# Optimization experiments

Measured on AMD Instinct MI355X. Metric: run time of the kernel, lower is better.

The kernel has to match this reference:

```python
import jax, jax.numpy as jnp
import numpy as np

NU, NM = 100000, 20000   # users, merchants
FU, FM = 64, 32          # input feature dims
H = 128                  # hidden_channels
E = 1000000              # edges per edge type
ET = 500000              # target edges


def setup_inputs() -> dict:
    key = jax.random.key(0)
    ks = jax.random.split(key, 24)
    f = lambda i, shape: jax.random.normal(ks[i], shape, jnp.float32) * 0.05
    ri = lambda i, n, hi: jax.random.randint(ks[i], (n,), 0, hi)
    return {
        'x_user': f(0, (NU, FU)),
        'x_merchant': f(1, (NM, FM)),
        'row_um': ri(2, E, NU), 'col_um': ri(3, E, NM),
        'row_mu': ri(4, E, NM), 'col_mu': ri(5, E, NU),
        'row_t': ri(6, ET, NU), 'col_t': ri(7, ET, NM),
        'W1l_um': f(8, (FU, H)), 'W1r_um': f(9, (FM, H)), 'b1_um': jnp.zeros((H,), jnp.float32),
        'W1l_mu': f(10, (FM, H)), 'W1r_mu': f(11, (FU, H)), 'b1_mu': jnp.zeros((H,), jnp.float32),
        'W2l_um': f(12, (H, H)), 'W2r_um': f(13, (H, H)), 'b2_um': jnp.zeros((H,), jnp.float32),
        'W2l_mu': f(14, (H, H)), 'W2r_mu': f(15, (H, H)), 'b2_mu': jnp.zeros((H,), jnp.float32),
        'Wc1': f(16, (2 * H, H)), 'bc1': jnp.zeros((H,), jnp.float32),
        'Wc2': f(17, (H, 1)), 'bc2': jnp.zeros((1,), jnp.float32),
    }


def _sage(x_src, x_dst, row, col, Wl, Wr, b, n_dst):
    # PyG SAGEConv (aggr='mean'): lin_l(mean of neighbor msgs) + lin_r(root) + bias
    deg = jax.ops.segment_sum(jnp.ones(row.shape[0], x_src.dtype), col, num_segments=n_dst)
    agg = jax.ops.segment_sum(x_src[row], col, num_segments=n_dst)
    agg = agg / jnp.maximum(deg, 1.0)[:, None]
    return agg @ Wl + x_dst @ Wr + b


def reference(x_user, x_merchant, row_um, col_um, row_mu, col_mu, row_t, col_t,
              W1l_um, W1r_um, b1_um, W1l_mu, W1r_mu, b1_mu,
              W2l_um, W2r_um, b2_um, W2l_mu, W2r_mu, b2_mu,
              Wc1, bc1, Wc2, bc2):
    # Layer 1 (each dest type receives exactly one edge type -> hetero-mean is identity)
    h_m = jax.nn.relu(_sage(x_user, x_merchant, row_um, col_um, W1l_um, W1r_um, b1_um, NM))
    h_u = jax.nn.relu(_sage(x_merchant, x_user, row_mu, col_mu, W1l_mu, W1r_mu, b1_mu, NU))
    # Layer 2 (no activation)
    z_m = _sage(h_u, h_m, row_um, col_um, W2l_um, W2r_um, b2_um, NM)
    z_u = _sage(h_m, h_u, row_mu, col_mu, W2l_mu, W2r_mu, b2_mu, NU)
    # Edge classifier: gather sender ('user') / receiver ('merchant'), concat, MLP
    z = jnp.concatenate([z_u[row_t], z_m[col_t]], axis=-1)  # [ET, 2H]
    h = jax.nn.relu(z @ Wc1 + bc1)
    return (h @ Wc2 + bc2).reshape(-1)
```

## Files before the change

### kernel.cpp

```cpp
#include <hip/hip_runtime.h>
#include <hip/hip_bf16.h>

#define NUV 100000
#define NMV 20000
#define NEV 1000000
#define ETV 500000

#define REP 8
#define SCH2 16384
#define NCA 10
#define NCB 49
#define HGRID 1954
#define MBLK 5000
#define G1MB 625
#define G2MB 313

typedef unsigned short u16;
typedef unsigned int u32;
typedef __attribute__((ext_vector_type(8))) short s16x8;
typedef __attribute__((ext_vector_type(4))) float f32x4;
typedef __attribute__((ext_vector_type(4))) unsigned short u16x4;
typedef __attribute__((ext_vector_type(4))) unsigned int u32x4;

__device__ inline u16 bf16r(float f) {
  u32 b = __builtin_bit_cast(u32, f);
  u32 r = b + 0x7fffu + ((b >> 16) & 1u);
  return (u16)(r >> 16);
}
__device__ inline float bflo(u32 v) { return __builtin_bit_cast(float, v << 16); }
__device__ inline float bfhi(u32 v) { return __builtin_bit_cast(float, v & 0xffff0000u); }

__device__ inline int xcc_id() {
  unsigned x;
  asm volatile("s_getreg_b32 %0, hwreg(HW_REG_XCC_ID, 0, 8)" : "=s"(x));
  return (int)(x & 7u);
}

#define GLOAD_LDS16(src, dst) \
  __builtin_amdgcn_global_load_lds((const __attribute__((address_space(1))) void*)(src), \
                                   (__attribute__((address_space(3))) void*)(dst), 16, 0, 0)

__global__ __launch_bounds__(256) void k_hist_rank_p(
    const int* __restrict__ col_um, int* __restrict__ cnt_um, int* __restrict__ rank_um,
    const int* __restrict__ col_mu, int* __restrict__ cnt_mu, int* __restrict__ rank_mu) {
  int i = (blockIdx.x * 256 + threadIdx.x) * 4;
  if (i >= 2 * NEV) return;
  int r = xcc_id();
  u32 rtag = (u32)r << 24;
  bool um = i < NEV;
  const int* col = um ? col_um : col_mu;
  int* cnt = um ? cnt_um : cnt_mu;
  int* rank = um ? rank_um : rank_mu;
  int lo = um ? i : i - NEV;
  int4 c = *(const int4*)(col + lo);
  u32 k0 = (u32)__hip_atomic_fetch_add(&cnt[c.x * REP + r], 1, __ATOMIC_RELAXED, __HIP_MEMORY_SCOPE_WORKGROUP);
  u32 k1 = (u32)__hip_atomic_fetch_add(&cnt[c.y * REP + r], 1, __ATOMIC_RELAXED, __HIP_MEMORY_SCOPE_WORKGROUP);
  u32 k2 = (u32)__hip_atomic_fetch_add(&cnt[c.z * REP + r], 1, __ATOMIC_RELAXED, __HIP_MEMORY_SCOPE_WORKGROUP);
  u32 k3 = (u32)__hip_atomic_fetch_add(&cnt[c.w * REP + r], 1, __ATOMIC_RELAXED, __HIP_MEMORY_SCOPE_WORKGROUP);
  int4 k;
  k.x = (int)(k0 | rtag); k.y = (int)(k1 | rtag);
  k.z = (int)(k2 | rtag); k.w = (int)(k3 | rtag);
  *(int4*)(rank + lo) = k;
}

__global__ __launch_bounds__(1024) void k_scan_p1(const int* __restrict__ cntA, int nA,
                                                  const int* __restrict__ cntB, int nB,
                                                  int* __restrict__ bsum) {
  int b = blockIdx.x;
  const int* arr; int n; int c;
  if (b < NCA) { arr = cntA; n = nA; c = b; }
  else         { arr = cntB; n = nB; c = b - NCA; }
  __shared__ int wsum[16];
  int tid = threadIdx.x, lane = tid & 63, w = tid >> 6;
  int base = c * SCH2 + tid * 16;
  int s = 0;
  #pragma unroll
  for (int q = 0; q < 16; q += 4) {
    if (base + q + 3 < n) {
      int4 v = *(const int4*)(arr + base + q);
      s += v.x + v.y + v.z + v.w;
    } else {
      #pragma unroll
      for (int j = 0; j < 4; ++j) s += (base + q + j < n) ? arr[base + q + j] : 0;
    }
  }
  #pragma unroll
  for (int d = 1; d < 64; d <<= 1) s += __shfl_xor(s, d);
  if (lane == 0) wsum[w] = s;
  __syncthreads();
  if (tid == 0) {
    int tot = 0;
    #pragma unroll
    for (int j = 0; j < 16; ++j) tot += wsum[j];
    bsum[b] = tot;
  }
}

__global__ __launch_bounds__(128) void k_scan_p2(int* __restrict__ bsum,
                                                 int* __restrict__ off_um, int* __restrict__ off_mu) {
  int tid = threadIdx.x;
  int wv = tid >> 6, lane = tid & 63;
  if (wv == 0) {
    int v = (lane < NCA) ? bsum[lane] : 0;
    int s = v;
    #pragma unroll
    for (int d = 1; d < 64; d <<= 1) { int t = __shfl_up(s, d); if (lane >= d) s += t; }
    if (lane < NCA) bsum[lane] = s - v;
  } else {
    int v = (lane < NCB) ? bsum[NCA + lane] : 0;
    int s = v;
    #pragma unroll
    for (int d = 1; d < 64; d <<= 1) { int t = __shfl_up(s, d); if (lane >= d) s += t; }
    if (lane < NCB) bsum[NCA + lane] = s - v;
  }
  if (tid == 0) { off_um[NMV] = NEV; off_mu[NUV] = NEV; }
}

__global__ __launch_bounds__(1024) void k_scan_p3(int* __restrict__ cntA, int nA, int* __restrict__ offA,
                                                  int* __restrict__ cntB, int nB, int* __restrict__ offB,
                                                  const int* __restrict__ bsum) {
  int b = blockIdx.x;
  int* arr; int n; int c; int* offo;
  if (b < NCA) { arr = cntA; n = nA; c = b; offo = offA; }
  else         { arr = cntB; n = nB; c = b - NCA; offo = offB; }
  int carry = bsum[b];
  __shared__ int wsum[16];
  int tid = threadIdx.x, lane = tid & 63, w = tid >> 6;
  int base = c * SCH2 + tid * 16;
  int v[16];
  #pragma unroll
  for (int q = 0; q < 16; q += 4) {
    if (base + q + 3 < n) {
      int4 t = *(const int4*)(arr + base + q);
      v[q] = t.x; v[q + 1] = t.y; v[q + 2] = t.z; v[q + 3] = t.w;
    } else {
      #pragma unroll
      for (int j = 0; j < 4; ++j) v[q + j] = (base + q + j < n) ? arr[base + q + j] : 0;
    }
  }
  int tsum = 0;
  #pragma unroll
  for (int q = 0; q < 16; ++q) tsum += v[q];
  int sc = tsum;
  #pragma unroll
  for (int d = 1; d < 64; d <<= 1) { int t = __shfl_up(sc, d); if (lane >= d) sc += t; }
  if (lane == 63) wsum[w] = sc;
  __syncthreads();
  if (w == 0 && lane < 16) {
    int ws_ = wsum[lane];
    #pragma unroll
    for (int d = 1; d < 16; d <<= 1) { int t = __shfl_up(ws_, d, 16); if (lane >= d) ws_ += t; }
    wsum[lane] = ws_;
  }
  __syncthreads();
  int run = sc - tsum + (w ? wsum[w - 1] : 0) + carry;
  #pragma unroll
  for (int q = 0; q < 16; ++q) {
    int idx = base + q;
    if (idx < n) {
      arr[idx] = run;
      if ((idx & (REP - 1)) == 0) offo[idx / REP] = run;
      run += v[q];
    }
  }
}

__global__ __launch_bounds__(256) void k_scatter2(
    const int* __restrict__ col_um, const int* __restrict__ row_um,
    const int* __restrict__ rank_um, const int* __restrict__ base_um, int* __restrict__ srow_um,
    const int* __restrict__ col_mu, const int* __restrict__ row_mu,
    const int* __restrict__ rank_mu, const int* __restrict__ base_mu, int* __restrict__ srow_mu) {
  int i = (blockIdx.x * 256 + threadIdx.x) * 4;
  if (i >= 2 * NEV) return;
  bool um = i < NEV;
  const int* col = um ? col_um : col_mu;
  const int* row = um ? row_um : row_mu;
  const int* rank = um ? rank_um : rank_mu;
  const int* basep = um ? base_um : base_mu;
  int* srow = um ? srow_um : srow_mu;
  int lo = um ? i : i - NEV;
  int4 c = *(const int4*)(col + lo);
  int4 rr = *(const int4*)(row + lo);
  int4 k = *(const int4*)(rank + lo);
  u32 kx = (u32)k.x, ky = (u32)k.y, kz = (u32)k.z, kw = (u32)k.w;
  srow[basep[c.x * REP + (kx >> 24)] + (int)(kx & 0xFFFFFF)] = rr.x;
  srow[basep[c.y * REP + (ky >> 24)] + (int)(ky & 0xFFFFFF)] = rr.y;
  srow[basep[c.z * REP + (kz >> 24)] + (int)(kz & 0xFFFFFF)] = rr.z;
  srow[basep[c.w * REP + (kw >> 24)] + (int)(kw & 0xFFFFFF)] = rr.w;
}

__global__ __launch_bounds__(256) void k_xub(const float* __restrict__ in, u32* __restrict__ o, int n8) {
  int stride = gridDim.x * 256;
  for (int i = blockIdx.x * 256 + threadIdx.x; i < n8; i += stride) {
    float4 a = *(const float4*)(in + (size_t)i * 8);
    float4 b = *(const float4*)(in + (size_t)i * 8 + 4);
    u32x4 r;
    r[0] = (u32)bf16r(a.x) | ((u32)bf16r(a.y) << 16);
    r[1] = (u32)bf16r(a.z) | ((u32)bf16r(a.w) << 16);
    r[2] = (u32)bf16r(b.x) | ((u32)bf16r(b.y) << 16);
    r[3] = (u32)bf16r(b.z) | ((u32)bf16r(b.w) << 16);
    *(u32x4*)(o + (size_t)i * 4) = r;
  }
}

__global__ __launch_bounds__(256) void k_agg_l1(
    const int* __restrict__ off_um, const int* __restrict__ srow_um,
    const u32* __restrict__ xub, float* __restrict__ agg_m,
    const int* __restrict__ off_mu, const int* __restrict__ srow_mu,
    const float* __restrict__ xm, float* __restrict__ agg_u) {
  int bid = blockIdx.x, tid = threadIdx.x;
  int l = tid & 63, g = l >> 3, lr = l & 7;
  if (bid < MBLK) {
    int wid = (bid * 256 + tid) >> 6;
    int s = off_um[wid], t = off_um[wid + 1];
    float a[8] = {};
    int j = s;
    for (; j + 16 <= t; j += 16) {
      int r0 = srow_um[j + g], r1 = srow_um[j + 8 + g];
      u32x4 v0 = *(const u32x4*)(xub + (size_t)r0 * 32 + lr * 4);
      u32x4 v1 = *(const u32x4*)(xub + (size_t)r1 * 32 + lr * 4);
      #pragma unroll
      for (int k = 0; k < 4; ++k) {
        a[2 * k] += bflo(v0[k]) + bflo(v1[k]);
        a[2 * k + 1] += bfhi(v0[k]) + bfhi(v1[k]);
      }
    }
    for (; j + 8 <= t; j += 8) {
      int r0 = srow_um[j + g];
      u32x4 v0 = *(const u32x4*)(xub + (size_t)r0 * 32 + lr * 4);
      #pragma unroll
      for (int k = 0; k < 4; ++k) { a[2 * k] += bflo(v0[k]); a[2 * k + 1] += bfhi(v0[k]); }
    }
    if (g < t - j) {
      int r0 = srow_um[j + g];
      u32x4 v0 = *(const u32x4*)(xub + (size_t)r0 * 32 + lr * 4);
      #pragma unroll
      for (int k = 0; k < 4; ++k) { a[2 * k] += bflo(v0[k]); a[2 * k + 1] += bfhi(v0[k]); }
    }
    #pragma unroll
    for (int k = 0; k < 8; ++k) {
      a[k] += __shfl_xor(a[k], 8);
      a[k] += __shfl_xor(a[k], 16);
      a[k] += __shfl_xor(a[k], 32);
    }
    if (g == 0) {
      float inv = 1.f / (float)max(t - s, 1);
      float4 o0 = make_float4(a[0] * inv, a[1] * inv, a[2] * inv, a[3] * inv);
      float4 o1 = make_float4(a[4] * inv, a[5] * inv, a[6] * inv, a[7] * inv);
      *(float4*)(agg_m + (size_t)wid * 64 + lr * 8) = o0;
      *(float4*)(agg_m + (size_t)wid * 64 + lr * 8 + 4) = o1;
    }
  } else {
    int wid = ((bid - MBLK) * 256 + tid) >> 6;
    int s = off_mu[wid], t = off_mu[wid + 1];
    float a[4] = {};
    int j = s;
    for (; j + 16 <= t; j += 16) {
      int r0 = srow_mu[j + g], r1 = srow_mu[j + 8 + g];
      float4 v0 = *(const float4*)(xm + (size_t)r0 * 32 + lr * 4);
      float4 v1 = *(const float4*)(xm + (size_t)r1 * 32 + lr * 4);
      a[0] += v0.x + v1.x; a[1] += v0.y + v1.y;
      a[2] += v0.z + v1.z; a[3] += v0.w + v1.w;
    }
    for (; j + 8 <= t; j += 8) {
      int r0 = srow_mu[j + g];
      float4 v0 = *(const float4*)(xm + (size_t)r0 * 32 + lr * 4);
      a[0] += v0.x; a[1] += v0.y; a[2] += v0.z; a[3] += v0.w;
    }
    if (g < t - j) {
      int r0 = srow_mu[j + g];
      float4 v0 = *(const float4*)(xm + (size_t)r0 * 32 + lr * 4);
      a[0] += v0.x; a[1] += v0.y; a[2] += v0.z; a[3] += v0.w;
    }
    #pragma unroll
    for (int k = 0; k < 4; ++k) {
      a[k] += __shfl_xor(a[k], 8);
      a[k] += __shfl_xor(a[k], 16);
      a[k] += __shfl_xor(a[k], 32);
    }
    if (g == 0) {
      float inv = 1.f / (float)max(t - s, 1);
      *(float4*)(agg_u + (size_t)wid * 32 + lr * 4) =
          make_float4(a[0] * inv, a[1] * inv, a[2] * inv, a[3] * inv);
    }
  }
}

__global__ __launch_bounds__(256) void k_agg_l2(
    const int* __restrict__ off_um, const int* __restrict__ srow_um,
    const u16* __restrict__ h_u, u16* __restrict__ aggb_m,
    const int* __restrict__ off_mu, const int* __restrict__ srow_mu,
    const u16* __restrict__ h_m, u16* __restrict__ aggb_u) {
  int bid = blockIdx.x, tid = threadIdx.x;
  const int* off; const int* srow; const u32* x; u32* ag; int wid;
  if (bid < MBLK) {
    off = off_um; srow = srow_um; x = (const u32*)h_u; ag = (u32*)aggb_m;
    wid = (bid * 256 + tid) >> 6;
  } else {
    off = off_mu; srow = srow_mu; x = (const u32*)h_m; ag = (u32*)aggb_u;
    wid = ((bid - MBLK) * 256 + tid) >> 6;
  }
  int l = tid & 63, g = l >> 4, lr = l & 15;
  int s = off[wid], t = off[wid + 1];
  float a[8] = {};
  int j = s;
  for (; j + 8 <= t; j += 8) {
    int r0 = srow[j + g], r1 = srow[j + 4 + g];
    u32x4 v0 = *(const u32x4*)(x + (size_t)r0 * 64 + lr * 4);
    u32x4 v1 = *(const u32x4*)(x + (size_t)r1 * 64 + lr * 4);
    #pragma unroll
    for (int k = 0; k < 4; ++k) {
      a[2 * k] += bflo(v0[k]) + bflo(v1[k]);
      a[2 * k + 1] += bfhi(v0[k]) + bfhi(v1[k]);
    }
  }
  for (; j + 4 <= t; j += 4) {
    int r0 = srow[j + g];
    u32x4 v0 = *(const u32x4*)(x + (size_t)r0 * 64 + lr * 4);
    #pragma unroll
    for (int k = 0; k < 4; ++k) { a[2 * k] += bflo(v0[k]); a[2 * k + 1] += bfhi(v0[k]); }
  }
  if (g < t - j) {
    int r0 = srow[j + g];
    u32x4 v0 = *(const u32x4*)(x + (size_t)r0 * 64 + lr * 4);
    #pragma unroll
    for (int k = 0; k < 4; ++k) { a[2 * k] += bflo(v0[k]); a[2 * k + 1] += bfhi(v0[k]); }
  }
  #pragma unroll
  for (int k = 0; k < 8; ++k) {
    a[k] += __shfl_xor(a[k], 16);
    a[k] += __shfl_xor(a[k], 32);
  }
  if (g == 0) {
    float inv = 1.f / (float)max(t - s, 1);
    u32x4 o;
    #pragma unroll
    for (int k = 0; k < 4; ++k)
      o[k] = (u32)bf16r(a[2 * k] * inv) | ((u32)bf16r(a[2 * k + 1] * inv) << 16);
    *(u32x4*)(ag + (size_t)wid * 64 + lr * 4) = o;
  }
}

template <int KA, int KB>
__device__ inline void gemm1_body(const float* __restrict__ A, const float* __restrict__ B,
                                  const float* __restrict__ Wa, const float* __restrict__ Wb,
                                  const float* __restrict__ bias, u16* __restrict__ outb,
                                  int m0, float* At, float* Bt) {
  int tid = threadIdx.x;
  {
    int m = tid & 31, kq = tid >> 5;
    const float* Ar = A + (size_t)(m0 + m) * KA;
    for (int k0 = kq * 4; k0 < KA; k0 += 32) {
      float4 v = *(const float4*)(Ar + k0);
      At[(k0 + 0) * 32 + m] = v.x; At[(k0 + 1) * 32 + m] = v.y;
      At[(k0 + 2) * 32 + m] = v.z; At[(k0 + 3) * 32 + m] = v.w;
    }
    const float* Br = B + (size_t)(m0 + m) * KB;
    for (int k0 = kq * 4; k0 < KB; k0 += 32) {
      float4 v = *(const float4*)(Br + k0);
      Bt[(k0 + 0) * 32 + m] = v.x; Bt[(k0 + 1) * 32 + m] = v.y;
      Bt[(k0 + 2) * 32 + m] = v.z; Bt[(k0 + 3) * 32 + m] = v.w;
    }
  }
  __syncthreads();
  int tx = tid & 31, ty = tid >> 5;
  float acc[4][4] = {};
  #pragma unroll 4
  for (int k = 0; k < KA; ++k) {
    float4 wv = *(const float4*)(Wa + k * 128 + tx * 4);
    float4 av = *(const float4*)(&At[k * 32 + ty * 4]);
    float am[4] = {av.x, av.y, av.z, av.w};
    float wo[4] = {wv.x, wv.y, wv.z, wv.w};
    #pragma unroll
    for (int mi = 0; mi < 4; ++mi)
      #pragma unroll
      for (int oi = 0; oi < 4; ++oi) acc[mi][oi] += am[mi] * wo[oi];
  }
  #pragma unroll 4
  for (int k = 0; k < KB; ++k) {
    float4 wv = *(const float4*)(Wb + k * 128 + tx * 4);
    float4 av = *(const float4*)(&Bt[k * 32 + ty * 4]);
    float am[4] = {av.x, av.y, av.z, av.w};
    float wo[4] = {wv.x, wv.y, wv.z, wv.w};
    #pragma unroll
    for (int mi = 0; mi < 4; ++mi)
      #pragma unroll
      for (int oi = 0; oi < 4; ++oi) acc[mi][oi] += am[mi] * wo[oi];
  }
  float4 bv = *(const float4*)(bias + tx * 4);
  float bb[4] = {bv.x, bv.y, bv.z, bv.w};
  #pragma unroll
  for (int mi = 0; mi < 4; ++mi) {
    u16x4 o;
    #pragma unroll
    for (int oi = 0; oi < 4; ++oi) {
      float v = acc[mi][oi] + bb[oi];
      v = v > 0.f ? v : 0.f;
      o[oi] = bf16r(v);
    }
    *(u16x4*)(outb + (size_t)(m0 + ty * 4 + mi) * 128 + tx * 4) = o;
  }
}

__global__ __launch_bounds__(256) void k_gemm1(
    const float* __restrict__ agg_m, const float* __restrict__ x_merch,
    const float* __restrict__ W1l_um, const float* __restrict__ W1r_um,
    const float* __restrict__ b1_um, u16* __restrict__ h_m,
    const float* __restrict__ agg_u, const float* __restrict__ x_user,
    const float* __restrict__ W1l_mu, const float* __restrict__ W1r_mu,
    const float* __restrict__ b1_mu, u16* __restrict__ h_u) {
  __shared__ float At[64 * 32];
  __shared__ float Bt[64 * 32];
  int bid = blockIdx.x;
  if (bid < G1MB)
    gemm1_body<64, 32>(agg_m, x_merch, W1l_um, W1r_um, b1_um, h_m, bid * 32, At, Bt);
  else
    gemm1_body<32, 64>(agg_u, x_user, W1l_mu, W1r_mu, b1_mu, h_u, (bid - G1MB) * 32, At, Bt);
}

__global__ __launch_bounds__(256) void k_prep_comb(
    const float* __restrict__ W2l_um, const float* __restrict__ W2r_um,
    const float* __restrict__ W2l_mu, const float* __restrict__ W2r_mu,
    const float* __restrict__ b2_um, const float* __restrict__ b2_mu,
    const float* __restrict__ Wc1, const float* __restrict__ bc1,
    u16* __restrict__ WtA_u, u16* __restrict__ WtB_u,
    u16* __restrict__ WtA_m, u16* __restrict__ WtB_m,
    float* __restrict__ bias_u, float* __restrict__ bias_m) {
  int t = blockIdx.x * 256 + threadIdx.x;
  if (t < 65536) {
    int mat = t >> 14, rem = t & 16383;
    int o = rem >> 7, k = rem & 127;
    const float* W2 = mat == 0 ? W2l_mu : mat == 1 ? W2r_mu : mat == 2 ? W2l_um : W2r_um;
    const float* wc = Wc1 + (mat >= 2 ? 128 * 128 : 0) + o;
    float s = 0.f;
    #pragma unroll 4
    for (int j = 0; j < 128; ++j) s += W2[k * 128 + j] * wc[j * 128];
    u16* dst = mat == 0 ? WtA_u : mat == 1 ? WtB_u : mat == 2 ? WtA_m : WtB_m;
    dst[o * 128 + k] = bf16r(s);
  } else if (t < 65536 + 256) {
    int r = t - 65536;
    int o = r & 127;
    if (r < 128) {
      float s = 0.f;
      for (int j = 0; j < 128; ++j) s += b2_mu[j] * Wc1[j * 128 + o];
      bias_u[o] = s;
    } else {
      float s = bc1[o];
      for (int j = 0; j < 128; ++j) s += b2_um[j] * Wc1[(128 + j) * 128 + o];
      bias_m[o] = s;
    }
  }
}

__global__ __launch_bounds__(256) void k_gemm2_mfma(
    const u16* __restrict__ aggb_m, const u16* __restrict__ h_m,
    const u16* __restrict__ WtA_m, const u16* __restrict__ WtB_m,
    const float* __restrict__ bias_m, u16* __restrict__ pm_b,
    const u16* __restrict__ aggb_u, const u16* __restrict__ h_u,
    const u16* __restrict__ WtA_u, const u16* __restrict__ WtB_u,
    const float* __restrict__ bias_u, u16* __restrict__ pu_b) {
  __shared__ u16 Zs[64 * 256];
  int tid = threadIdx.x;
  int bid = blockIdx.x;
  const u16 *aggb, *hb, *Wtl, *Wtr; const float* bias; u16* zb; int nd, r0;
  if (bid < G2MB) {
    aggb = aggb_m; hb = h_m; Wtl = WtA_m; Wtr = WtB_m; bias = bias_m; zb = pm_b;
    nd = NMV; r0 = bid * 64;
  } else {
    aggb = aggb_u; hb = h_u; Wtl = WtA_u; Wtr = WtB_u; bias = bias_u; zb = pu_b;
    nd = NUV; r0 = (bid - G2MB) * 64;
  }
  {
    int half = (tid >> 4) & 1;
    const u16* tab = half ? hb : aggb;
    #pragma unroll
    for (int it = 0; it < 8; ++it) {
      int q = tid + it * 256;
      int rl = q >> 5;
      int cc = (q & 15) ^ (rl & 7);
      int r = r0 + rl; r = r < nd ? r : nd - 1;
      const u16* src = tab + (size_t)r * 128 + cc * 8;
      u16* dst = Zs + (tid >> 6) * 512 + it * 2048;
      GLOAD_LDS16(src, dst);
    }
  }
  __syncthreads();
  int l = tid & 63, wv = tid >> 6;
  int lg = l >> 4, lr = l & 15;
  f32x4 acc[4][2];
  #pragma unroll
  for (int mt = 0; mt < 4; ++mt)
    #pragma unroll
    for (int c = 0; c < 2; ++c) acc[mt][c] = (f32x4){0.f, 0.f, 0.f, 0.f};
  #pragma unroll
  for (int cti = 0; cti < 2; ++cti) {
    int o = (wv * 2 + cti) * 16 + lr;
    const u16* wpl = Wtl + (size_t)o * 128 + lg * 8;
    const u16* wpr = Wtr + (size_t)o * 128 + lg * 8;
    s16x8 b[8];
    #pragma unroll
    for (int ks = 0; ks < 4; ++ks) b[ks] = *(const s16x8*)(wpl + ks * 32);
    #pragma unroll
    for (int ks = 0; ks < 4; ++ks) b[ks + 4] = *(const s16x8*)(wpr + ks * 32);
    #pragma unroll
    for (int mt = 0; mt < 4; ++mt) {
      int rl = mt * 16 + lr;
      int rb = rl * 512, sw = (rl & 7) << 4;
      #pragma unroll
      for (int ks = 0; ks < 8; ++ks) {
        s16x8 a = *(const s16x8*)((const char*)Zs + ((rb + ks * 64 + lg * 16) ^ sw));
        acc[mt][cti] = __builtin_amdgcn_mfma_f32_16x16x32_bf16(a, b[ks], acc[mt][cti], 0, 0, 0);
      }
    }
  }
  float bv[2];
  #pragma unroll
  for (int cti = 0; cti < 2; ++cti) bv[cti] = bias[(wv * 2 + cti) * 16 + lr];
  #pragma unroll
  for (int mt = 0; mt < 4; ++mt)
    #pragma unroll
    for (int cti = 0; cti < 2; ++cti) {
      int o = (wv * 2 + cti) * 16 + lr;
      #pragma unroll
      for (int rg = 0; rg < 4; ++rg) {
        int r = r0 + mt * 16 + lg * 4 + rg;
        if (r < nd) zb[(size_t)r * 128 + o] = bf16r(acc[mt][cti][rg] + bv[cti]);
      }
    }
}

__global__ __launch_bounds__(256) void k_edge(
    const u32* __restrict__ pu, const u32* __restrict__ pm,
    const int* __restrict__ row_t, const int* __restrict__ col_t,
    const float* __restrict__ Wc2, const float* __restrict__ bc2,
    float* __restrict__ out) {
  __shared__ float res[256];
  int tid = threadIdx.x, l = tid & 63, wv = tid >> 6;
  int lr = l & 15, g = l >> 4;
  float w2v[8];
  #pragma unroll
  for (int q = 0; q < 8; ++q) w2v[q] = Wc2[lr * 8 + q];
  int base = blockIdx.x * 256 + wv * 64;
  #pragma unroll 2
  for (int it = 0; it < 16; ++it) {
    int e = base + it * 4 + g;
    int ec = e < ETV ? e : ETV - 1;
    int r = row_t[ec], c = col_t[ec];
    u32x4 a = *(const u32x4*)(pu + (size_t)r * 64 + lr * 4);
    u32x4 b = *(const u32x4*)(pm + (size_t)c * 64 + lr * 4);
    float p = 0.f;
    #pragma unroll
    for (int q = 0; q < 4; ++q) {
      float h0 = bflo(a[q]) + bflo(b[q]);
      float h1 = bfhi(a[q]) + bfhi(b[q]);
      h0 = h0 > 0.f ? h0 : 0.f;
      h1 = h1 > 0.f ? h1 : 0.f;
      p += h0 * w2v[2 * q] + h1 * w2v[2 * q + 1];
    }
    p += __shfl_xor(p, 1); p += __shfl_xor(p, 2);
    p += __shfl_xor(p, 4); p += __shfl_xor(p, 8);
    if (lr == 0) res[wv * 64 + it * 4 + g] = p;
  }
  __syncthreads();
  int eo = blockIdx.x * 256 + tid;
  if (eo < ETV) out[eo] = res[tid] + bc2[0];
}

extern "C" void kernel_launch(void* const* d_in, const int* in_sizes, int n_in,
                              void* d_out, int out_size, void* d_ws, size_t ws_size,
                              hipStream_t stream) {
  const float* x_user  = (const float*)d_in[0];
  const float* x_merch = (const float*)d_in[1];
  const int* row_um = (const int*)d_in[2]; const int* col_um = (const int*)d_in[3];
  const int* row_mu = (const int*)d_in[4]; const int* col_mu = (const int*)d_in[5];
  const int* row_t  = (const int*)d_in[6]; const int* col_t  = (const int*)d_in[7];
  const float* W1l_um = (const float*)d_in[8];  const float* W1r_um = (const float*)d_in[9];  const float* b1_um = (const float*)d_in[10];
  const float* W1l_mu = (const float*)d_in[11]; const float* W1r_mu = (const float*)d_in[12]; const float* b1_mu = (const float*)d_in[13];
  const float* W2l_um = (const float*)d_in[14]; const float* W2r_um = (const float*)d_in[15]; const float* b2_um = (const float*)d_in[16];
  const float* W2l_mu = (const float*)d_in[17]; const float* W2r_mu = (const float*)d_in[18]; const float* b2_mu = (const float*)d_in[19];
  const float* Wc1 = (const float*)d_in[20]; const float* bc1 = (const float*)d_in[21];
  const float* Wc2 = (const float*)d_in[22]; const float* bc2 = (const float*)d_in[23];
  float* out = (float*)d_out;

  char* ws = (char*)d_ws;
  size_t p = 0;
  auto alloc = [&](size_t bytes) -> char* {
    char* r = ws + p;
    p = (p + bytes + 255) & ~(size_t)255;
    return r;
  };
  int* cnt_um = (int*)alloc((size_t)NMV * REP * 4);
  int* cnt_mu = (int*)alloc((size_t)NUV * REP * 4);
  size_t zero_end = p;
  int* off_um = (int*)alloc((size_t)(NMV + 1) * 4);
  int* off_mu = (int*)alloc((size_t)(NUV + 1) * 4);
  int* bsum = (int*)alloc((size_t)(NCA + NCB) * 4);
  int* rank_um = (int*)alloc((size_t)NEV * 4);
  int* rank_mu = (int*)alloc((size_t)NEV * 4);
  int* srow_um = (int*)alloc((size_t)NEV * 4);
  int* srow_mu = (int*)alloc((size_t)NEV * 4);
  u32* xub = (u32*)alloc((size_t)NUV * 32 * 4);
  float* agg_m = (float*)alloc((size_t)NMV * 64 * 4);
  float* agg_u = (float*)alloc((size_t)NUV * 32 * 4);
  u16* h_m   = (u16*)alloc((size_t)NMV * 128 * 2);
  u16* h_u   = (u16*)alloc((size_t)NUV * 128 * 2);
  u16* aggb_m = (u16*)alloc((size_t)NMV * 128 * 2);
  u16* aggb_u = (u16*)alloc((size_t)NUV * 128 * 2);
  u16* pm_b  = (u16*)alloc((size_t)NMV * 128 * 2);
  u16* pu_b  = (u16*)alloc((size_t)NUV * 128 * 2);
  u16* WtA_u = (u16*)alloc((size_t)128 * 128 * 2);
  u16* WtB_u = (u16*)alloc((size_t)128 * 128 * 2);
  u16* WtA_m = (u16*)alloc((size_t)128 * 128 * 2);
  u16* WtB_m = (u16*)alloc((size_t)128 * 128 * 2);
  float* bias_u = (float*)alloc(128 * 4);
  float* bias_m = (float*)alloc(128 * 4);
  if (p > ws_size) return;

  hipMemsetAsync(d_ws, 0, zero_end, stream);
  k_prep_comb<<<257, 256, 0, stream>>>(W2l_um, W2r_um, W2l_mu, W2r_mu, b2_um, b2_mu, Wc1, bc1,
                                       WtA_u, WtB_u, WtA_m, WtB_m, bias_u, bias_m);
  k_xub<<<1024, 256, 0, stream>>>(x_user, xub, NUV * 64 / 8);
  k_hist_rank_p<<<HGRID, 256, 0, stream>>>(col_um, cnt_um, rank_um, col_mu, cnt_mu, rank_mu);
  k_scan_p1<<<NCA + NCB, 1024, 0, stream>>>(cnt_um, NMV * REP, cnt_mu, NUV * REP, bsum);
  k_scan_p2<<<1, 128, 0, stream>>>(bsum, off_um, off_mu);
  k_scan_p3<<<NCA + NCB, 1024, 0, stream>>>(cnt_um, NMV * REP, off_um,
                                            cnt_mu, NUV * REP, off_mu, bsum);
  k_scatter2<<<HGRID, 256, 0, stream>>>(col_um, row_um, rank_um, cnt_um, srow_um,
                                        col_mu, row_mu, rank_mu, cnt_mu, srow_mu);
  k_agg_l1<<<MBLK + NUV / 4, 256, 0, stream>>>(off_um, srow_um, xub, agg_m,
                                               off_mu, srow_mu, x_merch, agg_u);
  k_gemm1<<<G1MB + NUV / 32, 256, 0, stream>>>(agg_m, x_merch, W1l_um, W1r_um, b1_um, h_m,
                                               agg_u, x_user, W1l_mu, W1r_mu, b1_mu, h_u);
  k_agg_l2<<<MBLK + NUV / 4, 256, 0, stream>>>(off_um, srow_um, h_u, aggb_m,
                                               off_mu, srow_mu, h_m, aggb_u);
  k_gemm2_mfma<<<G2MB + (NUV + 63) / 64, 256, 0, stream>>>(
      aggb_m, h_m, WtA_m, WtB_m, bias_m, pm_b,
      aggb_u, h_u, WtA_u, WtB_u, bias_u, pu_b);
  k_edge<<<(ETV + 255) / 256, 256, 0, stream>>>((const u32*)pu_b, (const u32*)pm_b,
                                                row_t, col_t, Wc2, bc2, out);
}
```

Measured before the change: 394.6 us.

## Store per-XCC degree counters in XCC-major planes and restructure CSR scan

The per-XCC replicated counters move from node-interleaved layout (node*8+xcc) to separate planes per XCC (xcc*N+node), so atomics from different XCCs no longer share cache lines. The scan becomes a reduce-across-planes pass writing per-node totals to a new buffer T, a scan over node totals, and a pass that writes exclusive offsets back into each plane. The histogram atomics also switch from workgroup-scoped fetch_add to device-scope atomicAdd, which may cost more per operation. The scatter index math is updated to the new layout.

```diff
diff --git a/kernel.cpp b/kernel.cpp
--- a/kernel.cpp
+++ b/kernel.cpp
@@ -7,9 +7,8 @@
 #define ETV 500000
 
 #define REP 8
-#define SCH2 16384
-#define NCA 10
-#define NCB 49
+#define NCA 5
+#define NCB 25
 #define HGRID 1954
 #define MBLK 5000
 #define G1MB 625
@@ -49,54 +48,53 @@
   u32 rtag = (u32)r << 24;
   bool um = i < NEV;
   const int* col = um ? col_um : col_mu;
-  int* cnt = um ? cnt_um : cnt_mu;
+  int* cnt = (um ? cnt_um : cnt_mu) + r * (um ? NMV : NUV);
   int* rank = um ? rank_um : rank_mu;
   int lo = um ? i : i - NEV;
   int4 c = *(const int4*)(col + lo);
-  u32 k0 = (u32)__hip_atomic_fetch_add(&cnt[c.x * REP + r], 1, __ATOMIC_RELAXED, __HIP_MEMORY_SCOPE_WORKGROUP);
-  u32 k1 = (u32)__hip_atomic_fetch_add(&cnt[c.y * REP + r], 1, __ATOMIC_RELAXED, __HIP_MEMORY_SCOPE_WORKGROUP);
-  u32 k2 = (u32)__hip_atomic_fetch_add(&cnt[c.z * REP + r], 1, __ATOMIC_RELAXED, __HIP_MEMORY_SCOPE_WORKGROUP);
-  u32 k3 = (u32)__hip_atomic_fetch_add(&cnt[c.w * REP + r], 1, __ATOMIC_RELAXED, __HIP_MEMORY_SCOPE_WORKGROUP);
+  u32 k0 = (u32)atomicAdd(&cnt[c.x], 1);
+  u32 k1 = (u32)atomicAdd(&cnt[c.y], 1);
+  u32 k2 = (u32)atomicAdd(&cnt[c.z], 1);
+  u32 k3 = (u32)atomicAdd(&cnt[c.w], 1);
   int4 k;
   k.x = (int)(k0 | rtag); k.y = (int)(k1 | rtag);
   k.z = (int)(k2 | rtag); k.w = (int)(k3 | rtag);
   *(int4*)(rank + lo) = k;
 }
 
-__global__ __launch_bounds__(1024) void k_scan_p1(const int* __restrict__ cntA, int nA,
-                                                  const int* __restrict__ cntB, int nB,
-                                                  int* __restrict__ bsum) {
+__global__ __launch_bounds__(1024) void k_scan_s1(const int* __restrict__ cnt_um,
+                                                  const int* __restrict__ cnt_mu,
+                                                  int* __restrict__ T, int* __restrict__ bsum) {
   int b = blockIdx.x;
-  const int* arr; int n; int c;
-  if (b < NCA) { arr = cntA; n = nA; c = b; }
-  else         { arr = cntB; n = nB; c = b - NCA; }
+  const int* cnt; int N; int c0; int* Tout;
+  if (b < NCA) { cnt = cnt_um; N = NMV; c0 = b * 4096; Tout = T; }
+  else         { cnt = cnt_mu; N = NUV; c0 = (b - NCA) * 4096; Tout = T + NMV; }
   __shared__ int wsum[16];
   int tid = threadIdx.x, lane = tid & 63, w = tid >> 6;
-  int base = c * SCH2 + tid * 16;
-  int s = 0;
-  #pragma unroll
-  for (int q = 0; q < 16; q += 4) {
-    if (base + q + 3 < n) {
-      int4 v = *(const int4*)(arr + base + q);
-      s += v.x + v.y + v.z + v.w;
-    } else {
-      #pragma unroll
-      for (int j = 0; j < 4; ++j) s += (base + q + j < n) ? arr[base + q + j] : 0;
-    }
-  }
-  #pragma unroll
-  for (int d = 1; d < 64; d <<= 1) s += __shfl_xor(s, d);
-  if (lane == 0) wsum[w] = s;
+  int c = c0 + tid * 4;
+  int4 s = make_int4(0, 0, 0, 0);
+  if (c < N) {
+    #pragma unroll
+    for (int r = 0; r < REP; ++r) {
+      int4 v = *(const int4*)(cnt + (size_t)r * N + c);
+      s.x += v.x; s.y += v.y; s.z += v.z; s.w += v.w;
+    }
+    *(int4*)(Tout + c) = s;
+  }
+  int tot = s.x + s.y + s.z + s.w;
+  #pragma unroll
+  for (int d = 1; d < 64; d <<= 1) tot += __shfl_xor(tot, d);
+  if (lane == 0) wsum[w] = tot;
   __syncthreads();
   if (tid == 0) {
-    int tot = 0;
-    #pragma unroll
-    for (int j = 0; j < 16; ++j) tot += wsum[j];
-    bsum[b] = tot;
-  }
-}
-
-__global__ __launch_bounds__(128) void k_scan_p2(int* __restrict__ bsum,
+    int a = 0;
+    #pragma unroll
+    for (int j = 0; j < 16; ++j) a += wsum[j];
+    bsum[b] = a;
+  }
+}
+
+__global__ __launch_bounds__(128) void k_scan_s2(int* __restrict__ bsum,
                                                  int* __restrict__ off_um, int* __restrict__ off_mu) {
   int tid = threadIdx.x;
   int wv = tid >> 6, lane = tid & 63;
@@ -116,32 +114,21 @@
   if (tid == 0) { off_um[NMV] = NEV; off_mu[NUV] = NEV; }
 }
 
-__global__ __launch_bounds__(1024) void k_scan_p3(int* __restrict__ cntA, int nA, int* __restrict__ offA,
-                                                  int* __restrict__ cntB, int nB, int* __restrict__ offB,
-                                                  const int* __restrict__ bsum) {
+__global__ __launch_bounds__(1024) void k_scan_s3(int* __restrict__ cnt_um, int* __restrict__ off_um,
+                                                  int* __restrict__ cnt_mu, int* __restrict__ off_mu,
+                                                  const int* __restrict__ T, const int* __restrict__ bsum) {
   int b = blockIdx.x;
-  int* arr; int n; int c; int* offo;
-  if (b < NCA) { arr = cntA; n = nA; c = b; offo = offA; }
-  else         { arr = cntB; n = nB; c = b - NCA; offo = offB; }
+  int* cnt; int N; int c0; int* offo; const int* Tin;
+  if (b < NCA) { cnt = cnt_um; N = NMV; c0 = b * 4096; offo = off_um; Tin = T; }
+  else         { cnt = cnt_mu; N = NUV; c0 = (b - NCA) * 4096; offo = off_mu; Tin = T + NMV; }
   int carry = bsum[b];
   __shared__ int wsum[16];
   int tid = threadIdx.x, lane = tid & 63, w = tid >> 6;
-  int base = c * SCH2 + tid * 16;
-  int v[16];
-  #pragma unroll
-  for (int q = 0; q < 16; q += 4) {
-    if (base + q + 3 < n) {
-      int4 t = *(const int4*)(arr + base + q);
-      v[q] = t.x; v[q + 1] = t.y; v[q + 2] = t.z; v[q + 3] = t.w;
-    } else {
-      #pragma unroll
-      for (int j = 0; j < 4; ++j) v[q + j] = (base + q + j < n) ? arr[base + q + j] : 0;
-    }
-  }
-  int tsum = 0;
-  #pragma unroll
-  for (int q = 0; q < 16; ++q) tsum += v[q];
-  int sc = tsum;
+  int c = c0 + tid * 4;
+  int4 tv = make_int4(0, 0, 0, 0);
+  if (c < N) tv = *(const int4*)(Tin + c);
+  int p1 = tv.x + tv.y, p2 = p1 + tv.z, p3 = p2 + tv.w;
+  int sc = p3;
   #pragma unroll
   for (int d = 1; d < 64; d <<= 1) { int t = __shfl_up(sc, d); if (lane >= d) sc += t; }
   if (lane == 63) wsum[w] = sc;
@@ -153,14 +140,15 @@
     wsum[lane] = ws_;
   }
   __syncthreads();
-  int run = sc - tsum + (w ? wsum[w - 1] : 0) + carry;
-  #pragma unroll
-  for (int q = 0; q < 16; ++q) {
-    int idx = base + q;
-    if (idx < n) {
-      arr[idx] = run;
-      if ((idx & (REP - 1)) == 0) offo[idx / REP] = run;
-      run += v[q];
+  int ex = sc - p3 + (w ? wsum[w - 1] : 0) + carry;
+  if (c < N) {
+    *(int4*)(offo + c) = make_int4(ex, ex + tv.x, ex + p1, ex + p2);
+    int4 run = make_int4(ex, ex + tv.x, ex + p1, ex + p2);
+    #pragma unroll
+    for (int r = 0; r < REP; ++r) {
+      int4 v = *(const int4*)(cnt + (size_t)r * N + c);
+      *(int4*)(cnt + (size_t)r * N + c) = run;
+      run.x += v.x; run.y += v.y; run.z += v.z; run.w += v.w;
     }
   }
 }
@@ -177,16 +165,17 @@
   const int* row = um ? row_um : row_mu;
   const int* rank = um ? rank_um : rank_mu;
   const int* basep = um ? base_um : base_mu;
+  int N = um ? NMV : NUV;
   int* srow = um ? srow_um : srow_mu;
   int lo = um ? i : i - NEV;
   int4 c = *(const int4*)(col + lo);
   int4 rr = *(const int4*)(row + lo);
   int4 k = *(const int4*)(rank + lo);
   u32 kx = (u32)k.x, ky = (u32)k.y, kz = (u32)k.z, kw = (u32)k.w;
-  srow[basep[c.x * REP + (kx >> 24)] + (int)(kx & 0xFFFFFF)] = rr.x;
-  srow[basep[c.y * REP + (ky >> 24)] + (int)(ky & 0xFFFFFF)] = rr.y;
-  srow[basep[c.z * REP + (kz >> 24)] + (int)(kz & 0xFFFFFF)] = rr.z;
-  srow[basep[c.w * REP + (kw >> 24)] + (int)(kw & 0xFFFFFF)] = rr.w;
+  srow[basep[(int)(kx >> 24) * N + c.x] + (int)(kx & 0xFFFFFF)] = rr.x;
+  srow[basep[(int)(ky >> 24) * N + c.y] + (int)(ky & 0xFFFFFF)] = rr.y;
+  srow[basep[(int)(kz >> 24) * N + c.z] + (int)(kz & 0xFFFFFF)] = rr.z;
+  srow[basep[(int)(kw >> 24) * N + c.w] + (int)(kw & 0xFFFFFF)] = rr.w;
 }
 
 __global__ __launch_bounds__(256) void k_xub(const float* __restrict__ in, u32* __restrict__ o, int n8) {
@@ -592,8 +581,9 @@
   int* cnt_um = (int*)alloc((size_t)NMV * REP * 4);
   int* cnt_mu = (int*)alloc((size_t)NUV * REP * 4);
   size_t zero_end = p;
-  int* off_um = (int*)alloc((size_t)(NMV + 1) * 4);
-  int* off_mu = (int*)alloc((size_t)(NUV + 1) * 4);
+  int* off_um = (int*)alloc((size_t)(NMV + 4) * 4);
+  int* off_mu = (int*)alloc((size_t)(NUV + 4) * 4);
+  int* T    = (int*)alloc((size_t)(NMV + NUV) * 4);
   int* bsum = (int*)alloc((size_t)(NCA + NCB) * 4);
   int* rank_um = (int*)alloc((size_t)NEV * 4);
   int* rank_mu = (int*)alloc((size_t)NEV * 4);
@@ -621,10 +611,9 @@
                                        WtA_u, WtB_u, WtA_m, WtB_m, bias_u, bias_m);
   k_xub<<<1024, 256, 0, stream>>>(x_user, xub, NUV * 64 / 8);
   k_hist_rank_p<<<HGRID, 256, 0, stream>>>(col_um, cnt_um, rank_um, col_mu, cnt_mu, rank_mu);
-  k_scan_p1<<<NCA + NCB, 1024, 0, stream>>>(cnt_um, NMV * REP, cnt_mu, NUV * REP, bsum);
-  k_scan_p2<<<1, 128, 0, stream>>>(bsum, off_um, off_mu);
-  k_scan_p3<<<NCA + NCB, 1024, 0, stream>>>(cnt_um, NMV * REP, off_um,
-                                            cnt_mu, NUV * REP, off_mu, bsum);
+  k_scan_s1<<<NCA + NCB, 1024, 0, stream>>>(cnt_um, cnt_mu, T, bsum);
+  k_scan_s2<<<1, 128, 0, stream>>>(bsum, off_um, off_mu);
+  k_scan_s3<<<NCA + NCB, 1024, 0, stream>>>(cnt_um, off_um, cnt_mu, off_mu, T, bsum);
   k_scatter2<<<HGRID, 256, 0, stream>>>(col_um, row_um, rank_um, cnt_um, srow_um,
                                         col_mu, row_mu, rank_mu, cnt_mu, srow_mu);
   k_agg_l1<<<MBLK + NUV / 4, 256, 0, stream>>>(off_um, srow_um, xub, agg_m,
```

New measurement: 377.2 us. -4.4%, faster.
